# Kernel optimization log

Hardware: AMD Instinct MI355X
Metric: run time of the kernel (lower is better)

The kernel has to match this reference:

```python
import jax, jax.numpy as jnp
import numpy as np

EPS = 1e-12  # matches tf.nn.l2_normalize epsilon used by keras backend


def l2n(x, axis):
    return x / jnp.sqrt(jnp.maximum(jnp.sum(x * x, axis=axis, keepdims=True), EPS))


def setup_inputs() -> dict:
    key = jax.random.key(0)
    k1, k2, k3 = jax.random.split(key, 3)
    B, T, D, P = 32, 256, 512, 20
    inp_a = jax.random.normal(k1, (B, T, D), dtype=jnp.float32)
    inp_b = jax.random.normal(k2, (B, T, D), dtype=jnp.float32)
    # build(): output_dim weights of shape (1, D), 'uniform' init -> stacked (P, D)
    W = jax.random.uniform(k3, (P, D), dtype=jnp.float32, minval=-0.05, maxval=0.05)
    return {"inp_a": inp_a, "inp_b": inp_b, "W": W}


def reference(inp_a, inp_b, W):
    # l2-normalize over feature dim
    na = l2n(inp_a, -1)  # (B,T,D)
    nb = l2n(inp_b, -1)  # (B,T,D)
    # K.batch_dot(outp_b, outp_a, axes=[1,1]): contract seq axis -> (B,D,D)
    alpha = jnp.einsum('btd,bte->bde', nb, na)
    alpha = l2n(alpha, 1)
    # K.batch_dot(outp_b, alpha, axes=[2,1]): contract feature axis of b with axis1 of alpha -> (B,T,D)
    hmean = jnp.einsum('btd,bde->bte', nb, alpha)
    # per-perspective weighting + l2-normalize, vectorized over P perspectives
    aw = l2n(inp_a[:, :, None, :] * W[None, None, :, :], -1)   # (B,T,P,D)
    hw = l2n(hmean[:, :, None, :] * W[None, None, :, :], -1)   # (B,T,P,D)
    # batch_dot(hw_i, aw_i, axes=[2,2]) * eye summed == rowwise dot (diagonal only)
    persp = jnp.sum(aw * hw, axis=-1)  # (B,T,P)
    return (persp, persp)
```

## Files before the change

### kernel.cpp

```cpp
#include <hip/hip_runtime.h>
#include <hip/hip_bf16.h>

#define BB 32
#define TT 256
#define DD 512
#define PP 20
#define EPSF 1e-12f
#define BTP (BB * TT * PP)

typedef __attribute__((ext_vector_type(8))) short short8;
typedef __attribute__((ext_vector_type(4))) float f32x4;

__device__ inline unsigned short f2bf(float f) {
    unsigned u = __float_as_uint(f);
    u += 0x7fffu + ((u >> 16) & 1u);
    return (unsigned short)(u >> 16);
}
__device__ inline unsigned pk2(float lo, float hi) {
    __hip_bfloat162 h = __float22bfloat162_rn(float2{lo, hi});
    union { __hip_bfloat162 h; unsigned u; } c;
    c.h = h;
    return c.u;
}
__device__ inline float bf2f(unsigned s) {
    return __uint_as_float(s << 16);
}

union U8 { short8 s; uint4 u; };

__global__ __launch_bounds__(256)
void k_prep(const float* __restrict__ a, const float* __restrict__ b,
            const float* __restrict__ W,
            unsigned short* __restrict__ na_bf,
            unsigned short* __restrict__ nb_bf,
            float* __restrict__ q, unsigned short* __restrict__ W2) {
    const int row  = blockIdx.x * 4 + (threadIdx.x >> 6);
    const int lane = threadIdx.x & 63;
    const float4* pa = (const float4*)(a + (size_t)row * DD);
    const float4* pb = (const float4*)(b + (size_t)row * DD);
    float4 a0 = pa[2 * lane], a1 = pa[2 * lane + 1];
    float4 b0 = pb[2 * lane], b1 = pb[2 * lane + 1];
    float sa = a0.x * a0.x + a0.y * a0.y + a0.z * a0.z + a0.w * a0.w
             + a1.x * a1.x + a1.y * a1.y + a1.z * a1.z + a1.w * a1.w;
    float sb = b0.x * b0.x + b0.y * b0.y + b0.z * b0.z + b0.w * b0.w
             + b1.x * b1.x + b1.y * b1.y + b1.z * b1.z + b1.w * b1.w;
#pragma unroll
    for (int off = 1; off < 64; off <<= 1) {
        sa += __shfl_xor(sa, off);
        sb += __shfl_xor(sb, off);
    }
    const float ia_ = rsqrtf(fmaxf(sa, EPSF));
    const float ib_ = rsqrtf(fmaxf(sb, EPSF));
    uint4 oa, ob;
    oa.x = pk2(a0.x * ia_, a0.y * ia_);
    oa.y = pk2(a0.z * ia_, a0.w * ia_);
    oa.z = pk2(a1.x * ia_, a1.y * ia_);
    oa.w = pk2(a1.z * ia_, a1.w * ia_);
    ob.x = pk2(b0.x * ib_, b0.y * ib_);
    ob.y = pk2(b0.z * ib_, b0.w * ib_);
    ob.z = pk2(b1.x * ib_, b1.y * ib_);
    ob.w = pk2(b1.z * ib_, b1.w * ib_);
    *(uint4*)(na_bf + (size_t)row * DD + 8 * lane) = oa;
    *(uint4*)(nb_bf + (size_t)row * DD + 8 * lane) = ob;
    if (lane < 2) {
        const int i2 = 2 * row + lane;
        q[i2] = 0.f;
        const float w = (i2 < PP * DD) ? W[i2] : 0.f;
        W2[i2] = f2bf(w * w);
    }
}

__global__ __launch_bounds__(256)
void k_gemm_g(const unsigned short* __restrict__ nb,
              unsigned short* __restrict__ G) {
    const int bz  = blockIdx.z;
    const int tid = threadIdx.x;
    const int t0 = blockIdx.y * 64;
    const int s0 = blockIdx.x * 64;
    __shared__ __align__(16) unsigned short As[64 * 40];
    __shared__ __align__(16) unsigned short Bs[64 * 40];

    const int wave = tid >> 6, lane = tid & 63;
    const int quad = lane >> 4, ln = lane & 15;
    const int wm = wave >> 1, wn = wave & 1;

    const unsigned short* nbb = nb + (size_t)bz * TT * DD;

    const int lr = tid >> 2;
    const int c8 = (tid & 3) * 8;

    f32x4 acc[2][2];
#pragma unroll
    for (int i = 0; i < 2; ++i)
#pragma unroll
        for (int j = 0; j < 2; ++j)
#pragma unroll
            for (int r = 0; r < 4; ++r) acc[i][j][r] = 0.f;

    for (int k0 = 0; k0 < DD; k0 += 32) {
        *(uint4*)&As[lr * 40 + c8] =
            *(const uint4*)(nbb + (size_t)(t0 + lr) * DD + k0 + c8);
        *(uint4*)&Bs[lr * 40 + c8] =
            *(const uint4*)(nbb + (size_t)(s0 + lr) * DD + k0 + c8);
        __syncthreads();
        short8 af[2], bf[2];
        af[0] = *(const short8*)&As[(wm * 32 + ln) * 40 + quad * 8];
        af[1] = *(const short8*)&As[(wm * 32 + 16 + ln) * 40 + quad * 8];
        bf[0] = *(const short8*)&Bs[(wn * 32 + ln) * 40 + quad * 8];
        bf[1] = *(const short8*)&Bs[(wn * 32 + 16 + ln) * 40 + quad * 8];
#pragma unroll
        for (int i = 0; i < 2; ++i)
#pragma unroll
            for (int j = 0; j < 2; ++j)
                acc[i][j] = __builtin_amdgcn_mfma_f32_16x16x32_bf16(
                    af[i], bf[j], acc[i][j], 0, 0, 0);
        __syncthreads();
    }
    unsigned short* Gb = G + (size_t)bz * TT * TT;
#pragma unroll
    for (int i = 0; i < 2; ++i)
#pragma unroll
        for (int j = 0; j < 2; ++j) {
            const int col = s0 + wn * 32 + j * 16 + ln;
            const int row0 = t0 + wm * 32 + i * 16 + quad * 4;
#pragma unroll
            for (int r = 0; r < 4; r += 2) {
                const unsigned pk = pk2(acc[i][j][r], acc[i][j][r + 1]);
                Gb[(size_t)(row0 + r) * TT + col] = (unsigned short)pk;
                Gb[(size_t)(row0 + r + 1) * TT + col] = (unsigned short)(pk >> 16);
            }
        }
}

__global__ __launch_bounds__(256)
void k_gemm_h(const unsigned short* __restrict__ G,
              const unsigned short* __restrict__ na,
              unsigned short* __restrict__ H, float* __restrict__ q) {
    const int bz = blockIdx.z;
    const int t0 = blockIdx.y * 64;
    const int e0 = blockIdx.x * 64;
    __shared__ __align__(16) unsigned short As[64 * 40];
    __shared__ __align__(16) unsigned short Bs[64 * 40];
    __shared__ float qsum[64];

    const int tid  = threadIdx.x;
    const int wave = tid >> 6, lane = tid & 63;
    const int quad = lane >> 4, ln = lane & 15;
    const int wm = wave >> 1, wn = wave & 1;

    const unsigned short* Gb  = G  + (size_t)bz * TT * TT;
    const unsigned short* nab = na + (size_t)bz * TT * DD;

    const int lr = tid >> 2;
    const int c8 = (tid & 3) * 8;
    const int kr = tid >> 3;
    const int e8 = (tid & 7) * 8;

    f32x4 acc[2][2];
#pragma unroll
    for (int i = 0; i < 2; ++i)
#pragma unroll
        for (int j = 0; j < 2; ++j)
#pragma unroll
            for (int r = 0; r < 4; ++r) acc[i][j][r] = 0.f;

    for (int k0 = 0; k0 < TT; k0 += 32) {
        *(uint4*)&As[lr * 40 + c8] =
            *(const uint4*)(Gb + (size_t)(t0 + lr) * TT + k0 + c8);
        {
            uint4 v = *(const uint4*)(nab + (size_t)(k0 + kr) * DD + e0 + e8);
            Bs[(e8 + 0) * 40 + kr] = (unsigned short)(v.x);
            Bs[(e8 + 1) * 40 + kr] = (unsigned short)(v.x >> 16);
            Bs[(e8 + 2) * 40 + kr] = (unsigned short)(v.y);
            Bs[(e8 + 3) * 40 + kr] = (unsigned short)(v.y >> 16);
            Bs[(e8 + 4) * 40 + kr] = (unsigned short)(v.z);
            Bs[(e8 + 5) * 40 + kr] = (unsigned short)(v.z >> 16);
            Bs[(e8 + 6) * 40 + kr] = (unsigned short)(v.w);
            Bs[(e8 + 7) * 40 + kr] = (unsigned short)(v.w >> 16);
        }
        __syncthreads();
        short8 af[2], bf[2];
        af[0] = *(const short8*)&As[(wm * 32 + ln) * 40 + quad * 8];
        af[1] = *(const short8*)&As[(wm * 32 + 16 + ln) * 40 + quad * 8];
        bf[0] = *(const short8*)&Bs[(wn * 32 + ln) * 40 + quad * 8];
        bf[1] = *(const short8*)&Bs[(wn * 32 + 16 + ln) * 40 + quad * 8];
#pragma unroll
        for (int i = 0; i < 2; ++i)
#pragma unroll
            for (int j = 0; j < 2; ++j)
                acc[i][j] = __builtin_amdgcn_mfma_f32_16x16x32_bf16(
                    af[i], bf[j], acc[i][j], 0, 0, 0);
        __syncthreads();
    }

    if (tid < 64) qsum[tid] = 0.f;
    __syncthreads();

    unsigned short* Hb = H + (size_t)bz * TT * DD;
#pragma unroll
    for (int j = 0; j < 2; ++j) {
        const int col = e0 + wn * 32 + j * 16 + ln;
        float qp = 0.f;
#pragma unroll
        for (int i = 0; i < 2; ++i) {
            const int row0 = t0 + wm * 32 + i * 16 + quad * 4;
#pragma unroll
            for (int r = 0; r < 4; r += 2) {
                const float hv0 = acc[i][j][r];
                const float hv1 = acc[i][j][r + 1];
                const unsigned pk = pk2(hv0, hv1);
                Hb[(size_t)(row0 + r) * DD + col] = (unsigned short)pk;
                Hb[(size_t)(row0 + r + 1) * DD + col] = (unsigned short)(pk >> 16);
                qp = fmaf(bf2f(nab[(size_t)(row0 + r) * DD + col]), hv0, qp);
                qp = fmaf(bf2f(nab[(size_t)(row0 + r + 1) * DD + col]), hv1, qp);
            }
        }
        qp += __shfl_xor(qp, 16);
        qp += __shfl_xor(qp, 32);
        if (quad == 0) atomicAdd(&qsum[wn * 32 + j * 16 + ln], qp);
    }
    __syncthreads();
    if (tid < 64) atomicAdd(q + bz * DD + e0 + tid, qsum[tid]);
}

__global__ __launch_bounds__(128)
void k_persp_mfma(const unsigned short* __restrict__ na,
                  const unsigned short* __restrict__ H,
                  const float* __restrict__ q,
                  const unsigned short* __restrict__ W2,
                  float* __restrict__ out) {
    const int b    = blockIdx.y;
    const int r0   = blockIdx.x * 16;
    const int wave = threadIdx.x >> 6;
    const int lane = threadIdx.x & 63;
    const int quad = lane >> 4, ln = lane & 15;
    const size_t rowbase = ((size_t)b * TT + r0 + ln) * DD;

    __shared__ float qs[DD];
    __shared__ float ps[64][24];
    {
        const float* qb = q + (size_t)b * DD;
        float4 v = *(const float4*)(qb + 4 * threadIdx.x);
        qs[4 * threadIdx.x + 0] = rsqrtf(fmaxf(v.x, EPSF));
        qs[4 * threadIdx.x + 1] = rsqrtf(fmaxf(v.y, EPSF));
        qs[4 * threadIdx.x + 2] = rsqrtf(fmaxf(v.z, EPSF));
        qs[4 * threadIdx.x + 3] = rsqrtf(fmaxf(v.w, EPSF));
    }
    __syncthreads();

    f32x4 s1[2], s2[2], s3[2];
#pragma unroll
    for (int j = 0; j < 2; ++j)
#pragma unroll
        for (int r = 0; r < 4; ++r) { s1[j][r] = 0.f; s2[j][r] = 0.f; s3[j][r] = 0.f; }

    const int kbeg = wave * 256;
    for (int k0 = kbeg; k0 < kbeg + 256; k0 += 32) {
        const int k = k0 + quad * 8;
        uint4 au = *(const uint4*)(na + rowbase + k);
        uint4 hu = *(const uint4*)(H + rowbase + k);
        float4 q0 = *(const float4*)&qs[k];
        float4 q1 = *(const float4*)&qs[k + 4];
        const float av[8] = {bf2f(au.x & 0xffffu), bf2f(au.x >> 16),
                             bf2f(au.y & 0xffffu), bf2f(au.y >> 16),
                             bf2f(au.z & 0xffffu), bf2f(au.z >> 16),
                             bf2f(au.w & 0xffffu), bf2f(au.w >> 16)};
        const float qv[8] = {q0.x, q0.y, q0.z, q0.w, q1.x, q1.y, q1.z, q1.w};
        float hv[8] = {bf2f(hu.x & 0xffffu), bf2f(hu.x >> 16),
                       bf2f(hu.y & 0xffffu), bf2f(hu.y >> 16),
                       bf2f(hu.z & 0xffffu), bf2f(hu.z >> 16),
                       bf2f(hu.w & 0xffffu), bf2f(hu.w >> 16)};
#pragma unroll
        for (int t = 0; t < 8; ++t) hv[t] *= qv[t];
        U8 ah, aa, hh;
        ah.u.x = pk2(av[0] * hv[0], av[1] * hv[1]);
        ah.u.y = pk2(av[2] * hv[2], av[3] * hv[3]);
        ah.u.z = pk2(av[4] * hv[4], av[5] * hv[5]);
        ah.u.w = pk2(av[6] * hv[6], av[7] * hv[7]);
        aa.u.x = pk2(av[0] * av[0], av[1] * av[1]);
        aa.u.y = pk2(av[2] * av[2], av[3] * av[3]);
        aa.u.z = pk2(av[4] * av[4], av[5] * av[5]);
        aa.u.w = pk2(av[6] * av[6], av[7] * av[7]);
        hh.u.x = pk2(hv[0] * hv[0], hv[1] * hv[1]);
        hh.u.y = pk2(hv[2] * hv[2], hv[3] * hv[3]);
        hh.u.z = pk2(hv[4] * hv[4], hv[5] * hv[5]);
        hh.u.w = pk2(hv[6] * hv[6], hv[7] * hv[7]);
        short8 bw0 = *(const short8*)(W2 + (size_t)ln * DD + k);
        short8 bw1 = *(const short8*)(W2 + (size_t)(16 + ln) * DD + k);
        s1[0] = __builtin_amdgcn_mfma_f32_16x16x32_bf16(ah.s, bw0, s1[0], 0, 0, 0);
        s1[1] = __builtin_amdgcn_mfma_f32_16x16x32_bf16(ah.s, bw1, s1[1], 0, 0, 0);
        s2[0] = __builtin_amdgcn_mfma_f32_16x16x32_bf16(aa.s, bw0, s2[0], 0, 0, 0);
        s2[1] = __builtin_amdgcn_mfma_f32_16x16x32_bf16(aa.s, bw1, s2[1], 0, 0, 0);
        s3[0] = __builtin_amdgcn_mfma_f32_16x16x32_bf16(hh.s, bw0, s3[0], 0, 0, 0);
        s3[1] = __builtin_amdgcn_mfma_f32_16x16x32_bf16(hh.s, bw1, s3[1], 0, 0, 0);
    }

    if (wave == 1) {
#pragma unroll
        for (int j = 0; j < 2; ++j)
#pragma unroll
            for (int r = 0; r < 4; ++r) {
                ps[lane][j * 4 + r]      = s1[j][r];
                ps[lane][8 + j * 4 + r]  = s2[j][r];
                ps[lane][16 + j * 4 + r] = s3[j][r];
            }
    }
    __syncthreads();
    if (wave == 0) {
#pragma unroll
        for (int j = 0; j < 2; ++j) {
            const int p = j * 16 + ln;
            if (p < PP) {
#pragma unroll
                for (int r = 0; r < 4; ++r) {
                    const float v1 = s1[j][r] + ps[lane][j * 4 + r];
                    const float v2 = s2[j][r] + ps[lane][8 + j * 4 + r];
                    const float v3 = s3[j][r] + ps[lane][16 + j * 4 + r];
                    const size_t row = (size_t)b * TT + r0 + quad * 4 + r;
                    const float v = v1 * rsqrtf(fmaxf(v2, EPSF))
                                       * rsqrtf(fmaxf(v3, EPSF));
                    out[row * PP + p] = v;
                    out[(size_t)BTP + row * PP + p] = v;
                }
            }
        }
    }
}

extern "C" void kernel_launch(void* const* d_in, const int* in_sizes, int n_in,
                              void* d_out, int out_size, void* d_ws, size_t ws_size,
                              hipStream_t stream) {
    (void)in_sizes; (void)n_in; (void)out_size; (void)ws_size;
    const float* a = (const float*)d_in[0];
    const float* b = (const float*)d_in[1];
    const float* W = (const float*)d_in[2];
    float* out = (float*)d_out;

    char* ws = (char*)d_ws;
    unsigned short* nb_bf = (unsigned short*)ws;
    unsigned short* na_bf = (unsigned short*)(ws + (8u << 20));
    unsigned short* G_bf  = (unsigned short*)(ws + (16u << 20));
    unsigned short* H_bf  = (unsigned short*)(ws + (20u << 20));
    float* q     = (float*)(ws + (28u << 20));
    unsigned short* W2 = (unsigned short*)(ws + (28u << 20) + (64u << 10));

    k_prep<<<BB * TT / 4, 256, 0, stream>>>(a, b, W, na_bf, nb_bf, q, W2);

    dim3 gG(4, 4, BB);
    k_gemm_g<<<gG, 256, 0, stream>>>(nb_bf, G_bf);

    dim3 gH(DD / 64, TT / 64, BB);
    k_gemm_h<<<gH, 256, 0, stream>>>(G_bf, na_bf, H_bf, q);

    dim3 gP(TT / 16, BB);
    k_persp_mfma<<<gP, 128, 0, stream>>>(na_bf, H_bf, q, W2, out);
}
```

Before: 110.2 us.

## Fuse Gram and H GEMMs into one kernel keeping G in shared memory

Merges the two GEMM kernels into one. Each block computes a 32-row strip of G = nb·nbᵀ against all 256 columns of its batch, keeps G in LDS, then multiplies it by na to produce H and accumulate q. The G intermediate no longer round-trips through global memory and one launch is dropped; global loads are register-prefetched one step ahead. The perspective kernel also moves to 4 waves with a split K reduction. The cost is heavy LDS use (about 58 KB per block), only 256 blocks, and every block reloading all of nb for its batch, which may lower occupancy.

Result: slower. 122.9 us (+11.6%).

```diff
diff --git a/kernel.cpp b/kernel.cpp
--- a/kernel.cpp
+++ b/kernel.cpp
@@ -71,159 +71,171 @@
 }
 
 __global__ __launch_bounds__(256)
-void k_gemm_g(const unsigned short* __restrict__ nb,
-              unsigned short* __restrict__ G) {
-    const int bz  = blockIdx.z;
+void k_gh(const unsigned short* __restrict__ nb,
+          const unsigned short* __restrict__ na,
+          unsigned short* __restrict__ H, float* __restrict__ q) {
+    const int bz  = blockIdx.y;
+    const int t0  = blockIdx.x * 32;
     const int tid = threadIdx.x;
-    const int t0 = blockIdx.y * 64;
-    const int s0 = blockIdx.x * 64;
-    __shared__ __align__(16) unsigned short As[64 * 40];
-    __shared__ __align__(16) unsigned short Bs[64 * 40];
-
     const int wave = tid >> 6, lane = tid & 63;
     const int quad = lane >> 4, ln = lane & 15;
-    const int wm = wave >> 1, wn = wave & 1;
+
+    __shared__ __align__(16) unsigned short Bs[512 * 40];
+    __shared__ __align__(16) unsigned short Gs[32 * 280];
 
     const unsigned short* nbb = nb + (size_t)bz * TT * DD;
+    const unsigned short* nab = na + (size_t)bz * TT * DD;
 
     const int lr = tid >> 2;
     const int c8 = (tid & 3) * 8;
 
-    f32x4 acc[2][2];
-#pragma unroll
-    for (int i = 0; i < 2; ++i)
-#pragma unroll
-        for (int j = 0; j < 2; ++j)
-#pragma unroll
-            for (int r = 0; r < 4; ++r) acc[i][j][r] = 0.f;
+    f32x4 acc1[2][4];
+#pragma unroll
+    for (int m = 0; m < 2; ++m)
+#pragma unroll
+        for (int n = 0; n < 4; ++n)
+#pragma unroll
+            for (int r = 0; r < 4; ++r) acc1[m][n][r] = 0.f;
+
+    uint4 cv1[4];
+#pragma unroll
+    for (int g = 0; g < 4; ++g)
+        cv1[g] = *(const uint4*)(nbb + (size_t)(g * 64 + lr) * DD + c8);
 
     for (int k0 = 0; k0 < DD; k0 += 32) {
-        *(uint4*)&As[lr * 40 + c8] =
-            *(const uint4*)(nbb + (size_t)(t0 + lr) * DD + k0 + c8);
-        *(uint4*)&Bs[lr * 40 + c8] =
-            *(const uint4*)(nbb + (size_t)(s0 + lr) * DD + k0 + c8);
+#pragma unroll
+        for (int g = 0; g < 4; ++g)
+            *(uint4*)&Bs[(g * 64 + lr) * 40 + c8] = cv1[g];
+        if (k0 + 32 < DD) {
+#pragma unroll
+            for (int g = 0; g < 4; ++g)
+                cv1[g] = *(const uint4*)(nbb + (size_t)(g * 64 + lr) * DD
+                                         + k0 + 32 + c8);
+        }
         __syncthreads();
-        short8 af[2], bf[2];
-        af[0] = *(const short8*)&As[(wm * 32 + ln) * 40 + quad * 8];
-        af[1] = *(const short8*)&As[(wm * 32 + 16 + ln) * 40 + quad * 8];
-        bf[0] = *(const short8*)&Bs[(wn * 32 + ln) * 40 + quad * 8];
-        bf[1] = *(const short8*)&Bs[(wn * 32 + 16 + ln) * 40 + quad * 8];
-#pragma unroll
-        for (int i = 0; i < 2; ++i)
-#pragma unroll
-            for (int j = 0; j < 2; ++j)
-                acc[i][j] = __builtin_amdgcn_mfma_f32_16x16x32_bf16(
-                    af[i], bf[j], acc[i][j], 0, 0, 0);
+        short8 af[2], bfr[4];
+        af[0] = *(const short8*)&Bs[(t0 + ln) * 40 + quad * 8];
+        af[1] = *(const short8*)&Bs[(t0 + 16 + ln) * 40 + quad * 8];
+#pragma unroll
+        for (int n = 0; n < 4; ++n)
+            bfr[n] = *(const short8*)&Bs[(wave * 64 + n * 16 + ln) * 40 + quad * 8];
+#pragma unroll
+        for (int m = 0; m < 2; ++m)
+#pragma unroll
+            for (int n = 0; n < 4; ++n)
+                acc1[m][n] = __builtin_amdgcn_mfma_f32_16x16x32_bf16(
+                    af[m], bfr[n], acc1[m][n], 0, 0, 0);
         __syncthreads();
     }
-    unsigned short* Gb = G + (size_t)bz * TT * TT;
-#pragma unroll
-    for (int i = 0; i < 2; ++i)
-#pragma unroll
-        for (int j = 0; j < 2; ++j) {
-            const int col = s0 + wn * 32 + j * 16 + ln;
-            const int row0 = t0 + wm * 32 + i * 16 + quad * 4;
+
+    const int eglow = tid & 3;
+    const int spair = (tid >> 2) & 15;
+    const int eghi  = tid >> 6;
+    uint4 cva[4], cvb[4];
+#pragma unroll
+    for (int g = 0; g < 4; ++g) {
+        const int eg = eglow + 4 * eghi + 16 * g;
+        const int s0 = 2 * spair;
+        cva[g] = *(const uint4*)(nab + (size_t)s0 * DD + eg * 8);
+        cvb[g] = *(const uint4*)(nab + (size_t)(s0 + 1) * DD + eg * 8);
+    }
+
+#pragma unroll
+    for (int m = 0; m < 2; ++m)
+#pragma unroll
+        for (int n = 0; n < 4; ++n) {
+            const int col = wave * 64 + n * 16 + ln;
+            const int row0 = m * 16 + quad * 4;
 #pragma unroll
             for (int r = 0; r < 4; r += 2) {
-                const unsigned pk = pk2(acc[i][j][r], acc[i][j][r + 1]);
-                Gb[(size_t)(row0 + r) * TT + col] = (unsigned short)pk;
-                Gb[(size_t)(row0 + r + 1) * TT + col] = (unsigned short)(pk >> 16);
-            }
-        }
-}
-
-__global__ __launch_bounds__(256)
-void k_gemm_h(const unsigned short* __restrict__ G,
-              const unsigned short* __restrict__ na,
-              unsigned short* __restrict__ H, float* __restrict__ q) {
-    const int bz = blockIdx.z;
-    const int t0 = blockIdx.y * 64;
-    const int e0 = blockIdx.x * 64;
-    __shared__ __align__(16) unsigned short As[64 * 40];
-    __shared__ __align__(16) unsigned short Bs[64 * 40];
-    __shared__ float qsum[64];
-
-    const int tid  = threadIdx.x;
-    const int wave = tid >> 6, lane = tid & 63;
-    const int quad = lane >> 4, ln = lane & 15;
-    const int wm = wave >> 1, wn = wave & 1;
-
-    const unsigned short* Gb  = G  + (size_t)bz * TT * TT;
-    const unsigned short* nab = na + (size_t)bz * TT * DD;
-
-    const int lr = tid >> 2;
-    const int c8 = (tid & 3) * 8;
-    const int kr = tid >> 3;
-    const int e8 = (tid & 7) * 8;
-
-    f32x4 acc[2][2];
-#pragma unroll
-    for (int i = 0; i < 2; ++i)
-#pragma unroll
-        for (int j = 0; j < 2; ++j)
-#pragma unroll
-            for (int r = 0; r < 4; ++r) acc[i][j][r] = 0.f;
-
+                const unsigned pk = pk2(acc1[m][n][r], acc1[m][n][r + 1]);
+                Gs[(row0 + r) * 280 + col] = (unsigned short)pk;
+                Gs[(row0 + r + 1) * 280 + col] = (unsigned short)(pk >> 16);
+            }
+        }
+    __syncthreads();
+
+    f32x4 acc2[2][8];
+#pragma unroll
+    for (int m = 0; m < 2; ++m)
+#pragma unroll
+        for (int n = 0; n < 8; ++n)
+#pragma unroll
+            for (int r = 0; r < 4; ++r) acc2[m][n][r] = 0.f;
+
+    unsigned* bp = (unsigned*)Bs;
     for (int k0 = 0; k0 < TT; k0 += 32) {
-        *(uint4*)&As[lr * 40 + c8] =
-            *(const uint4*)(Gb + (size_t)(t0 + lr) * TT + k0 + c8);
-        {
-            uint4 v = *(const uint4*)(nab + (size_t)(k0 + kr) * DD + e0 + e8);
-            Bs[(e8 + 0) * 40 + kr] = (unsigned short)(v.x);
-            Bs[(e8 + 1) * 40 + kr] = (unsigned short)(v.x >> 16);
-            Bs[(e8 + 2) * 40 + kr] = (unsigned short)(v.y);
-            Bs[(e8 + 3) * 40 + kr] = (unsigned short)(v.y >> 16);
-            Bs[(e8 + 4) * 40 + kr] = (unsigned short)(v.z);
-            Bs[(e8 + 5) * 40 + kr] = (unsigned short)(v.z >> 16);
-            Bs[(e8 + 6) * 40 + kr] = (unsigned short)(v.w);
-            Bs[(e8 + 7) * 40 + kr] = (unsigned short)(v.w >> 16);
+#pragma unroll
+        for (int g = 0; g < 4; ++g) {
+            const int eg = eglow + 4 * eghi + 16 * g;
+            const int base = eg * 160 + spair;
+            unsigned lo, hi;
+            lo = cva[g].x; hi = cvb[g].x;
+            bp[base +   0] = (lo & 0xffffu) | (hi << 16);
+            bp[base +  20] = (lo >> 16) | (hi & 0xffff0000u);
+            lo = cva[g].y; hi = cvb[g].y;
+            bp[base +  40] = (lo & 0xffffu) | (hi << 16);
+            bp[base +  60] = (lo >> 16) | (hi & 0xffff0000u);
+            lo = cva[g].z; hi = cvb[g].z;
+            bp[base +  80] = (lo & 0xffffu) | (hi << 16);
+            bp[base + 100] = (lo >> 16) | (hi & 0xffff0000u);
+            lo = cva[g].w; hi = cvb[g].w;
+            bp[base + 120] = (lo & 0xffffu) | (hi << 16);
+            bp[base + 140] = (lo >> 16) | (hi & 0xffff0000u);
+        }
+        if (k0 + 32 < TT) {
+#pragma unroll
+            for (int g = 0; g < 4; ++g) {
+                const int eg = eglow + 4 * eghi + 16 * g;
+                const int s0 = k0 + 32 + 2 * spair;
+                cva[g] = *(const uint4*)(nab + (size_t)s0 * DD + eg * 8);
+                cvb[g] = *(const uint4*)(nab + (size_t)(s0 + 1) * DD + eg * 8);
+            }
         }
         __syncthreads();
-        short8 af[2], bf[2];
-        af[0] = *(const short8*)&As[(wm * 32 + ln) * 40 + quad * 8];
-        af[1] = *(const short8*)&As[(wm * 32 + 16 + ln) * 40 + quad * 8];
-        bf[0] = *(const short8*)&Bs[(wn * 32 + ln) * 40 + quad * 8];
-        bf[1] = *(const short8*)&Bs[(wn * 32 + 16 + ln) * 40 + quad * 8];
-#pragma unroll
-        for (int i = 0; i < 2; ++i)
-#pragma unroll
-            for (int j = 0; j < 2; ++j)
-                acc[i][j] = __builtin_amdgcn_mfma_f32_16x16x32_bf16(
-                    af[i], bf[j], acc[i][j], 0, 0, 0);
+        short8 af2[2], bfr[8];
+#pragma unroll
+        for (int m = 0; m < 2; ++m)
+            af2[m] = *(const short8*)&Gs[(m * 16 + ln) * 280 + k0 + quad * 8];
+#pragma unroll
+        for (int n = 0; n < 8; ++n)
+            bfr[n] = *(const short8*)&Bs[(wave * 128 + n * 16 + ln) * 40 + quad * 8];
+#pragma unroll
+        for (int m = 0; m < 2; ++m)
+#pragma unroll
+            for (int n = 0; n < 8; ++n)
+                acc2[m][n] = __builtin_amdgcn_mfma_f32_16x16x32_bf16(
+                    af2[m], bfr[n], acc2[m][n], 0, 0, 0);
         __syncthreads();
     }
 
-    if (tid < 64) qsum[tid] = 0.f;
-    __syncthreads();
-
     unsigned short* Hb = H + (size_t)bz * TT * DD;
-#pragma unroll
-    for (int j = 0; j < 2; ++j) {
-        const int col = e0 + wn * 32 + j * 16 + ln;
+    float* qb = q + (size_t)bz * DD;
+#pragma unroll
+    for (int n = 0; n < 8; ++n) {
+        const int col = wave * 128 + n * 16 + ln;
         float qp = 0.f;
 #pragma unroll
-        for (int i = 0; i < 2; ++i) {
-            const int row0 = t0 + wm * 32 + i * 16 + quad * 4;
+        for (int m = 0; m < 2; ++m) {
+            const int row0 = t0 + m * 16 + quad * 4;
 #pragma unroll
             for (int r = 0; r < 4; r += 2) {
-                const float hv0 = acc[i][j][r];
-                const float hv1 = acc[i][j][r + 1];
-                const unsigned pk = pk2(hv0, hv1);
+                const float h0 = acc2[m][n][r];
+                const float h1 = acc2[m][n][r + 1];
+                const unsigned pk = pk2(h0, h1);
                 Hb[(size_t)(row0 + r) * DD + col] = (unsigned short)pk;
                 Hb[(size_t)(row0 + r + 1) * DD + col] = (unsigned short)(pk >> 16);
-                qp = fmaf(bf2f(nab[(size_t)(row0 + r) * DD + col]), hv0, qp);
-                qp = fmaf(bf2f(nab[(size_t)(row0 + r + 1) * DD + col]), hv1, qp);
+                qp = fmaf(bf2f(nab[(size_t)(row0 + r) * DD + col]), h0, qp);
+                qp = fmaf(bf2f(nab[(size_t)(row0 + r + 1) * DD + col]), h1, qp);
             }
         }
         qp += __shfl_xor(qp, 16);
         qp += __shfl_xor(qp, 32);
-        if (quad == 0) atomicAdd(&qsum[wn * 32 + j * 16 + ln], qp);
-    }
-    __syncthreads();
-    if (tid < 64) atomicAdd(q + bz * DD + e0 + tid, qsum[tid]);
-}
-
-__global__ __launch_bounds__(128)
+        if (quad == 0) atomicAdd(qb + col, qp);
+    }
+}
+
+__global__ __launch_bounds__(256)
 void k_persp_mfma(const unsigned short* __restrict__ na,
                   const unsigned short* __restrict__ H,
                   const float* __restrict__ q,
@@ -237,14 +249,12 @@
     const size_t rowbase = ((size_t)b * TT + r0 + ln) * DD;
 
     __shared__ float qs[DD];
-    __shared__ float ps[64][24];
+    __shared__ float ps[3][64][24];
     {
         const float* qb = q + (size_t)b * DD;
-        float4 v = *(const float4*)(qb + 4 * threadIdx.x);
-        qs[4 * threadIdx.x + 0] = rsqrtf(fmaxf(v.x, EPSF));
-        qs[4 * threadIdx.x + 1] = rsqrtf(fmaxf(v.y, EPSF));
-        qs[4 * threadIdx.x + 2] = rsqrtf(fmaxf(v.z, EPSF));
-        qs[4 * threadIdx.x + 3] = rsqrtf(fmaxf(v.w, EPSF));
+        float2 v = *(const float2*)(qb + 2 * threadIdx.x);
+        qs[2 * threadIdx.x + 0] = rsqrtf(fmaxf(v.x, EPSF));
+        qs[2 * threadIdx.x + 1] = rsqrtf(fmaxf(v.y, EPSF));
     }
     __syncthreads();
 
@@ -254,8 +264,8 @@
 #pragma unroll
         for (int r = 0; r < 4; ++r) { s1[j][r] = 0.f; s2[j][r] = 0.f; s3[j][r] = 0.f; }
 
-    const int kbeg = wave * 256;
-    for (int k0 = kbeg; k0 < kbeg + 256; k0 += 32) {
+    const int kbeg = wave * 128;
+    for (int k0 = kbeg; k0 < kbeg + 128; k0 += 32) {
         const int k = k0 + quad * 8;
         uint4 au = *(const uint4*)(na + rowbase + k);
         uint4 hu = *(const uint4*)(H + rowbase + k);
@@ -295,14 +305,14 @@
         s3[1] = __builtin_amdgcn_mfma_f32_16x16x32_bf16(hh.s, bw1, s3[1], 0, 0, 0);
     }
 
-    if (wave == 1) {
+    if (wave >= 1) {
 #pragma unroll
         for (int j = 0; j < 2; ++j)
 #pragma unroll
             for (int r = 0; r < 4; ++r) {
-                ps[lane][j * 4 + r]      = s1[j][r];
-                ps[lane][8 + j * 4 + r]  = s2[j][r];
-                ps[lane][16 + j * 4 + r] = s3[j][r];
+                ps[wave - 1][lane][j * 4 + r]      = s1[j][r];
+                ps[wave - 1][lane][8 + j * 4 + r]  = s2[j][r];
+                ps[wave - 1][lane][16 + j * 4 + r] = s3[j][r];
             }
     }
     __syncthreads();
@@ -313,9 +323,12 @@
             if (p < PP) {
 #pragma unroll
                 for (int r = 0; r < 4; ++r) {
-                    const float v1 = s1[j][r] + ps[lane][j * 4 + r];
-                    const float v2 = s2[j][r] + ps[lane][8 + j * 4 + r];
-                    const float v3 = s3[j][r] + ps[lane][16 + j * 4 + r];
+                    const float v1 = s1[j][r] + ps[0][lane][j * 4 + r]
+                                   + ps[1][lane][j * 4 + r] + ps[2][lane][j * 4 + r];
+                    const float v2 = s2[j][r] + ps[0][lane][8 + j * 4 + r]
+                                   + ps[1][lane][8 + j * 4 + r] + ps[2][lane][8 + j * 4 + r];
+                    const float v3 = s3[j][r] + ps[0][lane][16 + j * 4 + r]
+                                   + ps[1][lane][16 + j * 4 + r] + ps[2][lane][16 + j * 4 + r];
                     const size_t row = (size_t)b * TT + r0 + quad * 4 + r;
                     const float v = v1 * rsqrtf(fmaxf(v2, EPSF))
                                        * rsqrtf(fmaxf(v3, EPSF));
@@ -339,19 +352,15 @@
     char* ws = (char*)d_ws;
     unsigned short* nb_bf = (unsigned short*)ws;
     unsigned short* na_bf = (unsigned short*)(ws + (8u << 20));
-    unsigned short* G_bf  = (unsigned short*)(ws + (16u << 20));
-    unsigned short* H_bf  = (unsigned short*)(ws + (20u << 20));
-    float* q     = (float*)(ws + (28u << 20));
-    unsigned short* W2 = (unsigned short*)(ws + (28u << 20) + (64u << 10));
+    unsigned short* H_bf  = (unsigned short*)(ws + (16u << 20));
+    float* q     = (float*)(ws + (24u << 20));
+    unsigned short* W2 = (unsigned short*)(ws + (24u << 20) + (64u << 10));
 
     k_prep<<<BB * TT / 4, 256, 0, stream>>>(a, b, W, na_bf, nb_bf, q, W2);
 
-    dim3 gG(4, 4, BB);
-    k_gemm_g<<<gG, 256, 0, stream>>>(nb_bf, G_bf);
-
-    dim3 gH(DD / 64, TT / 64, BB);
-    k_gemm_h<<<gH, 256, 0, stream>>>(G_bf, na_bf, H_bf, q);
+    dim3 gGH(TT / 32, BB);
+    k_gh<<<gGH, 256, 0, stream>>>(nb_bf, na_bf, H_bf, q);
 
     dim3 gP(TT / 16, BB);
-    k_persp_mfma<<<gP, 128, 0, stream>>>(na_bf, H_bf, q, W2, out);
-}
+    k_persp_mfma<<<gP, 256, 0, stream>>>(na_bf, H_bf, q, W2, out);
+}
```
